# Optimization experiments

Measured on AMD Instinct MI355X. Metric: run time of the kernel, lower is better.

## Reference

```python
import jax, jax.numpy as jnp
import numpy as np

B, I, H, NC, T = 128, 256, 512, 16, 24
M = 14            # max ACT ticks (forward default M=14)
EPS = 0.01        # eps_halting default


def setup_inputs() -> dict:
    key = jax.random.key(0)
    ks = jax.random.split(key, 9)
    s = 1.0 / np.sqrt(H).astype(np.float32)
    u = lambda k, shape: jax.random.uniform(k, shape, jnp.float32, -s, s)
    return {
        "x": jax.random.normal(ks[0], (B, I, T), jnp.float32),
        # LSTMCell params, torch gate order (i, f, g, o)
        "W_ih": u(ks[1], (4 * H, I)),
        "W_hh": u(ks[2], (4 * H, H)),
        "b_ih": u(ks[3], (4 * H,)),
        "b_hh": u(ks[4], (4 * H,)),
        "halt_w": u(ks[5], (1, H)),
        "halt_b": u(ks[6], (1,)),
        "dec_w": u(ks[7], (NC, H)),
        "dec_b": u(ks[8], (NC,)),
    }


def _forward(x, W_ih, W_hh, b_ih, b_hh, halt_w, halt_b, dec_w, dec_b):
    Bn = x.shape[0]
    Hn = W_hh.shape[1]

    def lstm_cell(xi, h, c):
        g = xi @ W_ih.T + b_ih + h @ W_hh.T + b_hh
        i, f, gg, o = jnp.split(g, 4, axis=-1)
        c = jax.nn.sigmoid(f) * c + jax.nn.sigmoid(i) * jnp.tanh(gg)
        h = jax.nn.sigmoid(o) * jnp.tanh(c)
        return h, c

    def act_step(carry, xi):
        # Run M ticks; ACT weighting (ph) zeroes contributions past the halt step,
        # exactly reproducing the torch early-exit semantics.
        def tick(sc, _):
            h, c = lstm_cell(xi, sc[0], sc[1])
            pn = jax.nn.sigmoid(h @ halt_w.T + halt_b)[:, 0]  # [B]
            y = h @ dec_w.T + dec_b                            # [B, NC]
            return (h, c), (pn, h, c, y)

        _, (p_hist, s_hist, c_hist, y_hist) = jax.lax.scan(tick, carry, None, length=M)
        # p_hist [M,B]; s/c_hist [M,B,H]; y_hist [M,B,NC]
        pt_cum = jnp.cumsum(p_hist, axis=0)                    # [M,B]
        all_halted = jnp.all(pt_cum >= 1.0 - EPS, axis=1)      # [M]
        n_stop = jnp.where(jnp.any(all_halted), jnp.argmax(all_halted) + 1, M)
        idx = jnp.arange(M)[:, None]
        # torch: p_max = min(1, cumsum); p_max[:, -1] = 1.0 (last executed tick)
        p_max = jnp.where(idx >= n_stop - 1, 1.0, jnp.minimum(1.0, pt_cum))
        ph = jnp.concatenate([p_max[:1], jnp.diff(p_max, axis=0)], axis=0)  # [M,B]
        st = jnp.einsum('mb,mbh->bh', ph, s_hist)
        ct = jnp.einsum('mb,mbh->bh', ph, c_hist)
        yt = jnp.einsum('mb,mbc->bc', ph, y_hist)
        nt = jnp.argmax(p_max, axis=0)                         # [B] first tick hitting 1.0
        rt = 1.0 - p_max[nt - 1, jnp.arange(Bn)]               # negative index wraps like torch
        pt = nt.astype(x.dtype) + rt
        return (st, ct), (yt, pt, nt)

    z = jnp.zeros((Bn, Hn), x.dtype)
    _, (Y, P, N) = jax.lax.scan(act_step, (z, z), jnp.moveaxis(x, -1, 0))
    Y = jnp.moveaxis(Y, 0, -1)     # [B, NC, T]
    P = jnp.sum(P, axis=0)         # [B]
    N = N.T                        # [B, T]
    return Y, P, N


def reference(x, W_ih, W_hh, b_ih, b_hh, halt_w, halt_b, dec_w, dec_b):
    return _forward(x, W_ih, W_hh, b_ih, b_hh, halt_w, halt_b, dec_w, dec_b)
```

## Files before the change

kernel.cpp:

```cpp
#include <hip/hip_runtime.h>
#include <math.h>

#define NWG 256
#define TPB 1024

static constexpr int Bc=128, Ic=256, Hc=512, NCc=16, Tc=24, Mc=14;
static constexpr int Y_SZ  = Bc*NCc*Tc;
static constexpr int P_OFF = Y_SZ;
static constexpr int N_OFF = Y_SZ + Bc;

static constexpr int HSZ    = Hc*Bc;
static constexpr int HB_OFF = 0;
static constexpr int SC_OFF = 2*HSZ;
static constexpr int HP_OFF = 4*HSZ;
static constexpr int DP_OFF = HP_OFF + 2*2048;

typedef float f4v __attribute__((ext_vector_type(4)));

__device__ __align__(64) unsigned g_bcnt[16][16];
__device__ __align__(64) unsigned g_bgen[16][16];
__device__ __align__(64) unsigned g_brc[16];
__device__ __align__(64) unsigned g_brg[16];

__device__ __forceinline__ float sigm(float v){ return 1.0f/(1.0f+expf(-v)); }

__device__ __forceinline__ void gstore(float* p, float v){
  __hip_atomic_store(p, v, __ATOMIC_RELAXED, __HIP_MEMORY_SCOPE_SYSTEM);
}
__device__ __forceinline__ float gload(const float* p){
  return *(const volatile float*)p;
}

__device__ __forceinline__ void gsync(int w){
  __syncthreads();
  if (threadIdx.x == 0) {
    asm volatile("" ::: "memory");
    const int g = w >> 4;
    unsigned prev = __hip_atomic_fetch_add(&g_bcnt[g][0], 1u, __ATOMIC_RELAXED, __HIP_MEMORY_SCOPE_SYSTEM);
    unsigned ep   = prev >> 4;
    if ((prev & 15u) == 15u) {
      unsigned rprev = __hip_atomic_fetch_add(&g_brc[0], 1u, __ATOMIC_RELAXED, __HIP_MEMORY_SCOPE_SYSTEM);
      if ((rprev & 15u) == 15u) {
        __hip_atomic_store(&g_brg[0], (rprev >> 4) + 1u, __ATOMIC_RELEASE, __HIP_MEMORY_SCOPE_SYSTEM);
      } else {
        while ((int)(__hip_atomic_load(&g_brg[0], __ATOMIC_RELAXED, __HIP_MEMORY_SCOPE_SYSTEM) - (ep + 1u)) < 0)
          __builtin_amdgcn_s_sleep(1);
      }
      __hip_atomic_store(&g_bgen[g][0], ep + 1u, __ATOMIC_RELEASE, __HIP_MEMORY_SCOPE_SYSTEM);
    } else {
      while ((int)(__hip_atomic_load(&g_bgen[g][0], __ATOMIC_RELAXED, __HIP_MEMORY_SCOPE_SYSTEM) - (ep + 1u)) < 0)
        __builtin_amdgcn_s_sleep(1);
    }
    asm volatile("" ::: "memory");
  }
  __syncthreads();
}

__global__ __launch_bounds__(TPB, 1) void act_lstm_kernel(
    const float* __restrict__ x,   const float* __restrict__ Wih,
    const float* __restrict__ Whh, const float* __restrict__ bih,
    const float* __restrict__ bhh, const float* __restrict__ hw,
    const float* __restrict__ hbp, const float* __restrict__ dw,
    const float* __restrict__ db,  float* __restrict__ out,
    float* __restrict__ ws)
{
  const int w    = blockIdx.x;
  const int tid  = threadIdx.x;
  const int lane = tid & 63;
  const int wid  = __builtin_amdgcn_readfirstlane(tid >> 6);
  const int bg   = w >> 4;
  const int js   = w & 15;
  const int kg   = wid;
  const int rl0  = lane, rl1 = lane + 64;
  const int grow0 = ((rl0>>5)<<9) + js*32 + (rl0&31);
  const int grow1 = ((rl1>>5)<<9) + js*32 + (rl1&31);
  const bool iscell = (tid < 256);
  const int jloc = tid >> 3, bl = tid & 7;
  const int jglob = js*32 + jloc;
  const int bglob = bg*8 + bl;

  float* hbuf = ws + HB_OFF;
  float* stc  = ws + SC_OFF;
  float* hpp  = ws + HP_OFF;
  float* decp = ws + DP_OFF;

  __shared__ float h_lds[4096];
  __shared__ float x_lds[2048];
  __shared__ float part[128*129];
  __shared__ float sums[1024];
  __shared__ float dp[4096];
  __shared__ float hp[256];
  __shared__ float pmh[128];
  __shared__ float hq[2048];
  __shared__ float pnl[128];
  __shared__ float dy[2048];
  __shared__ unsigned ldsu[2];

  const f4v* Wh0 = (const f4v*)(Whh + grow0*Hc) + kg*8;
  const f4v* Wh1 = (const f4v*)(Whh + grow1*Hc) + kg*8;
  const f4v* Wx0 = (const f4v*)(Wih + grow0*Ic) + kg*4;
  const f4v* Wx1 = (const f4v*)(Wih + grow1*Ic) + kg*4;

  float bsum[4] = {0,0,0,0};
  float hwj = 0.f;
  if (iscell) {
    #pragma unroll
    for (int g=0; g<4; ++g) bsum[g] = bih[g*512 + jglob] + bhh[g*512 + jglob];
    hwj = hw[jglob];
  }
  const float hb0 = hbp[0];

  float c = 0.f, st_run = 0.f, ct_run = 0.f, prev_pm = 0.f;
  float cumw=0.f, prevw=0.f, ntfw=0.f, rtvw=0.f, psumw=0.f;
  bool  ntsetw = false;
  int   gt = 0, lastpar = 0, pend_t = -1, pend_par = 0;
  float xg[4] = {0,0,0,0};

  for (int t = 0; t < Tc; ++t) {
    for (int mm = 0;; ++mm) {
      const bool do_h = !(mm == 0 && t == 0);
      float xv0 = 0.f, xv1 = 0.f;
      if (mm == 0) {
        const int i0 = tid >> 3, b0 = tid & 7;
        const int xb = (bg*8 + b0) * (Ic*Tc);
        xv0 = x[xb + i0*Tc + t];
        xv1 = x[xb + (i0+128)*Tc + t];
      }
      if (do_h) {
        const float* src = (mm == 0) ? (stc + lastpar*HSZ) : (hbuf + ((gt-1)&1)*HSZ);
        const int j = tid >> 1, q = tid & 1;
        f4v hv = *(const volatile f4v*)(src + j*128 + bg*8 + q*4);
        *(f4v*)&h_lds[tid*4] = hv;
      }
      __syncthreads();

      if (mm == 0) {
        x_lds[tid]        = xv0;
        x_lds[tid + 1024] = xv1;
        __syncthreads();
        float a0[8] = {0,0,0,0,0,0,0,0}, a1[8] = {0,0,0,0,0,0,0,0};
        #pragma unroll
        for (int c4 = 0; c4 < 4; ++c4) {
          f4v w0 = Wx0[c4], w1 = Wx1[c4];
          #pragma unroll
          for (int d = 0; d < 4; ++d) {
            const float wa = w0[d], wb = w1[d];
            const float* hbp_ = &x_lds[(kg*16 + c4*4 + d)*8];
            f4v hA = *(const f4v*)hbp_, hB = *(const f4v*)(hbp_+4);
            a0[0]=fmaf(wa,hA.x,a0[0]); a0[1]=fmaf(wa,hA.y,a0[1]);
            a0[2]=fmaf(wa,hA.z,a0[2]); a0[3]=fmaf(wa,hA.w,a0[3]);
            a0[4]=fmaf(wa,hB.x,a0[4]); a0[5]=fmaf(wa,hB.y,a0[5]);
            a0[6]=fmaf(wa,hB.z,a0[6]); a0[7]=fmaf(wa,hB.w,a0[7]);
            a1[0]=fmaf(wb,hA.x,a1[0]); a1[1]=fmaf(wb,hA.y,a1[1]);
            a1[2]=fmaf(wb,hA.z,a1[2]); a1[3]=fmaf(wb,hA.w,a1[3]);
            a1[4]=fmaf(wb,hB.x,a1[4]); a1[5]=fmaf(wb,hB.y,a1[5]);
            a1[6]=fmaf(wb,hB.z,a1[6]); a1[7]=fmaf(wb,hB.w,a1[7]);
          }
        }
        #pragma unroll
        for (int b = 0; b < 8; ++b) {
          part[rl0*129 + kg*8 + b] = a0[b];
          part[rl1*129 + kg*8 + b] = a1[b];
        }
        __syncthreads();
        {
          const int row = tid >> 3, b = tid & 7;
          float s = 0.f;
          #pragma unroll
          for (int q2 = 0; q2 < 16; ++q2) s += part[row*129 + q2*8 + b];
          sums[tid] = s;
        }
        __syncthreads();
        if (iscell) {
          #pragma unroll
          for (int g = 0; g < 4; ++g) xg[g] = bsum[g] + sums[(g*32 + jloc)*8 + bl];
        }
        __syncthreads();
      }

      {
        float a0[8] = {0,0,0,0,0,0,0,0}, a1[8] = {0,0,0,0,0,0,0,0};
        if (do_h) {
          #pragma unroll
          for (int c4 = 0; c4 < 8; ++c4) {
            f4v w0 = Wh0[c4], w1 = Wh1[c4];
            #pragma unroll
            for (int d = 0; d < 4; ++d) {
              const float wa = w0[d], wb = w1[d];
              const float* hbp_ = &h_lds[(kg*32 + c4*4 + d)*8];
              f4v hA = *(const f4v*)hbp_, hB = *(const f4v*)(hbp_+4);
              a0[0]=fmaf(wa,hA.x,a0[0]); a0[1]=fmaf(wa,hA.y,a0[1]);
              a0[2]=fmaf(wa,hA.z,a0[2]); a0[3]=fmaf(wa,hA.w,a0[3]);
              a0[4]=fmaf(wa,hB.x,a0[4]); a0[5]=fmaf(wa,hB.y,a0[5]);
              a0[6]=fmaf(wa,hB.z,a0[6]); a0[7]=fmaf(wa,hB.w,a0[7]);
              a1[0]=fmaf(wb,hA.x,a1[0]); a1[1]=fmaf(wb,hA.y,a1[1]);
              a1[2]=fmaf(wb,hA.z,a1[2]); a1[3]=fmaf(wb,hA.w,a1[3]);
              a1[4]=fmaf(wb,hB.x,a1[4]); a1[5]=fmaf(wb,hB.y,a1[5]);
              a1[6]=fmaf(wb,hB.z,a1[6]); a1[7]=fmaf(wb,hB.w,a1[7]);
            }
          }
        }
        #pragma unroll
        for (int b = 0; b < 8; ++b) {
          part[rl0*129 + kg*8 + b] = a0[b];
          part[rl1*129 + kg*8 + b] = a1[b];
        }
      }
      __syncthreads();
      {
        const int row = tid >> 3, b = tid & 7;
        float s = 0.f;
        #pragma unroll
        for (int q2 = 0; q2 < 16; ++q2) s += part[row*129 + q2*8 + b];
        sums[tid] = s;
      }
      __syncthreads();

      float hn = 0.f, cn = 0.f;
      if (iscell) {
        float g0 = xg[0] + sums[(0*32 + jloc)*8 + bl];
        float g1 = xg[1] + sums[(1*32 + jloc)*8 + bl];
        float g2 = xg[2] + sums[(2*32 + jloc)*8 + bl];
        float g3 = xg[3] + sums[(3*32 + jloc)*8 + bl];
        float ig = sigm(g0), fg = sigm(g1), gg = tanhf(g2), og = sigm(g3);
        cn = fg*c + ig*gg;
        hn = og*tanhf(cn);
        const int par = gt & 1;
        gstore(hbuf + par*HSZ + jglob*128 + bglob, hn);
        gstore(stc  + par*HSZ + jglob*128 + bglob, st_run + (1.f - prev_pm)*hn);
        hp[tid] = hn * hwj;
      }
      __syncthreads();
      if (tid < 8) {
        float s = 0.f;
        #pragma unroll
        for (int jl = 0; jl < 32; ++jl) s += hp[jl*8 + tid];
        gstore(hpp + (gt&1)*2048 + js*128 + bg*8 + tid, s);
      }

      gsync(w);

      if (pend_t >= 0) {
        if (js == 0) {
          if (tid < 512) {
            const int js2 = tid >> 5, nc = (tid >> 1) & 15, hf = tid & 1;
            f4v v = *(const volatile f4v*)(decp + pend_par*32768 + js2*2048 + nc*128 + bg*8 + hf*4);
            *(f4v*)&dy[js2*128 + nc*8 + hf*4] = v;
          }
          __syncthreads();
          if (tid < 128) {
            const int nc = tid >> 3, b2 = tid & 7;
            float y = 0.f;
            #pragma unroll
            for (int js2 = 0; js2 < 16; ++js2) y += dy[js2*128 + nc*8 + b2];
            out[((bg*8 + b2)*NCc + nc)*Tc + pend_t] = y + db[nc];
          }
        }
        pend_t = -1;
      }
      const int par = gt & 1;
      if (tid < 512) {
        f4v v = *(const volatile f4v*)(hpp + par*2048 + tid*4);
        *(f4v*)&hq[tid*4] = v;
      }
      __syncthreads();
      if (tid < 128) {
        float s = 0.f;
        #pragma unroll
        for (int js2 = 0; js2 < 16; ++js2) s += hq[js2*128 + tid];
        pnl[tid] = s;
      }
      __syncthreads();
      if (wid < 2) {
        const int b2 = wid*64 + lane;
        float pn = sigm(pnl[b2] + hb0);
        cumw += pn;
        int ok = __all(cumw >= 0.99f) ? 1 : 0;
        if (lane == 0) ldsu[wid] = (unsigned)ok;
        pmh[b2] = fminf(1.f, cumw);
      }
      __syncthreads();
      const int finv = (((ldsu[0] & ldsu[1]) != 0u) || (mm == Mc-1)) ? 1 : 0;

      if (wid < 2) {
        float pmf = finv ? 1.f : fminf(1.f, cumw);
        if (!ntsetw && pmf >= 1.f) {
          ntfw = (float)mm;
          rtvw = (mm == 0) ? 0.f : (1.f - prevw);
          ntsetw = true;
        }
        prevw = pmf;
      }
      if (iscell) {
        float pm = finv ? 1.f : pmh[bglob];
        float ph = pm - prev_pm;
        st_run += ph*hn;
        ct_run += ph*cn;
        prev_pm = pm;
        c = finv ? ct_run : cn;
      }
      if (finv) {
        if (iscell) {
          #pragma unroll
          for (int nc = 0; nc < 16; ++nc)
            dp[nc*256 + tid] = dw[nc*512 + jglob] * st_run;
        }
        __syncthreads();
        if (tid < 128) {
          const int nc = tid >> 3, b2 = tid & 7;
          float s = 0.f;
          #pragma unroll
          for (int jl = 0; jl < 32; ++jl) s += dp[nc*256 + jl*8 + b2];
          gstore(decp + par*32768 + js*2048 + nc*128 + bg*8 + b2, s);
        }
        if (w == 0 && wid < 2)
          out[N_OFF + (wid*64 + lane)*Tc + t] = ntfw;
        if (wid < 2) {
          psumw += ntfw + rtvw;
          ntsetw = false; prevw = 0.f; cumw = 0.f; ntfw = 0.f; rtvw = 0.f;
        }
        if (iscell) { st_run = 0.f; ct_run = 0.f; prev_pm = 0.f; }
        pend_t = t; pend_par = par; lastpar = par;
      }
      ++gt;
      if (finv) break;
    }
  }

  gsync(w);
  if (pend_t >= 0 && js == 0) {
    if (tid < 512) {
      const int js2 = tid >> 5, nc = (tid >> 1) & 15, hf = tid & 1;
      f4v v = *(const volatile f4v*)(decp + pend_par*32768 + js2*2048 + nc*128 + bg*8 + hf*4);
      *(f4v*)&dy[js2*128 + nc*8 + hf*4] = v;
    }
    __syncthreads();
    if (tid < 128) {
      const int nc = tid >> 3, b2 = tid & 7;
      float y = 0.f;
      #pragma unroll
      for (int js2 = 0; js2 < 16; ++js2) y += dy[js2*128 + nc*8 + b2];
      out[((bg*8 + b2)*NCc + nc)*Tc + pend_t] = y + db[nc];
    }
  }
  if (w == 1 && wid < 2) out[P_OFF + wid*64 + lane] = psumw;
}

extern "C" void kernel_launch(void* const* d_in, const int* in_sizes, int n_in,
                              void* d_out, int out_size, void* d_ws, size_t ws_size,
                              hipStream_t stream) {
  const float* x   = (const float*)d_in[0];
  const float* Wih = (const float*)d_in[1];
  const float* Whh = (const float*)d_in[2];
  const float* bih = (const float*)d_in[3];
  const float* bhh = (const float*)d_in[4];
  const float* hw  = (const float*)d_in[5];
  const float* hb  = (const float*)d_in[6];
  const float* dwp = (const float*)d_in[7];
  const float* dbp = (const float*)d_in[8];
  float* out = (float*)d_out;
  float* ws  = (float*)d_ws;

  void* kargs[] = {(void*)&x, (void*)&Wih, (void*)&Whh, (void*)&bih, (void*)&bhh,
                   (void*)&hw, (void*)&hb, (void*)&dwp, (void*)&dbp, (void*)&out, (void*)&ws};
  hipLaunchCooperativeKernel((void*)act_lstm_kernel, dim3(NWG), dim3(TPB),
                             kargs, 0, stream);
}
```

Before: 1.998 ms.

## Remap workgroups across XCDs, prefetch hidden state after barrier, distribute decoder reduction

Changes the workgroup-to-(batch group, column slice) mapping so that consecutive block IDs, which land on different XCDs, spread the column slices across dies. Right after the grid barrier, each block loads the freshly written hidden-state slice into a register and reuses it as the next tick's h input, which removes the separate global load at the top of the next tick. The deferred decoder output reduction is now split so every block sums only its own class across the 16 column partials, instead of block js==0 reducing all 16 classes. This spreads the reduction work and removes one __syncthreads on that path, at the cost of an extra global read per tick that is wasted when the step halts.

```diff
diff --git a/kernel.cpp b/kernel.cpp
--- a/kernel.cpp
+++ b/kernel.cpp
@@ -68,8 +68,9 @@
   const int tid  = threadIdx.x;
   const int lane = tid & 63;
   const int wid  = __builtin_amdgcn_readfirstlane(tid >> 6);
-  const int bg   = w >> 4;
-  const int js   = w & 15;
+  const int xcg  = w & 7, xidx = w >> 3;
+  const int js   = (xcg << 1) | (xidx & 1);
+  const int bg   = xidx >> 1;
   const int kg   = wid;
   const int rl0  = lane, rl1 = lane + 64;
   const int grow0 = ((rl0>>5)<<9) + js*32 + (rl0&31);
@@ -93,7 +94,7 @@
   __shared__ float pmh[128];
   __shared__ float hq[2048];
   __shared__ float pnl[128];
-  __shared__ float dy[2048];
+  __shared__ float dy[128];
   __shared__ unsigned ldsu[2];
 
   const f4v* Wh0 = (const f4v*)(Whh + grow0*Hc) + kg*8;
@@ -115,6 +116,8 @@
   bool  ntsetw = false;
   int   gt = 0, lastpar = 0, pend_t = -1, pend_par = 0;
   float xg[4] = {0,0,0,0};
+  f4v   spec = {0,0,0,0};
+  bool  have_spec = false;
 
   for (int t = 0; t < Tc; ++t) {
     for (int mm = 0;; ++mm) {
@@ -127,10 +130,14 @@
         xv1 = x[xb + (i0+128)*Tc + t];
       }
       if (do_h) {
-        const float* src = (mm == 0) ? (stc + lastpar*HSZ) : (hbuf + ((gt-1)&1)*HSZ);
-        const int j = tid >> 1, q = tid & 1;
-        f4v hv = *(const volatile f4v*)(src + j*128 + bg*8 + q*4);
-        *(f4v*)&h_lds[tid*4] = hv;
+        if (mm > 0 && have_spec) {
+          *(f4v*)&h_lds[tid*4] = spec;
+        } else {
+          const float* src = (mm == 0) ? (stc + lastpar*HSZ) : (hbuf + ((gt-1)&1)*HSZ);
+          const int j = tid >> 1, q = tid & 1;
+          f4v hv = *(const volatile f4v*)(src + j*128 + bg*8 + q*4);
+          *(f4v*)&h_lds[tid*4] = hv;
+        }
       }
       __syncthreads();
 
@@ -240,28 +247,19 @@
 
       gsync(w);
 
-      if (pend_t >= 0) {
-        if (js == 0) {
-          if (tid < 512) {
-            const int js2 = tid >> 5, nc = (tid >> 1) & 15, hf = tid & 1;
-            f4v v = *(const volatile f4v*)(decp + pend_par*32768 + js2*2048 + nc*128 + bg*8 + hf*4);
-            *(f4v*)&dy[js2*128 + nc*8 + hf*4] = v;
-          }
-          __syncthreads();
-          if (tid < 128) {
-            const int nc = tid >> 3, b2 = tid & 7;
-            float y = 0.f;
-            #pragma unroll
-            for (int js2 = 0; js2 < 16; ++js2) y += dy[js2*128 + nc*8 + b2];
-            out[((bg*8 + b2)*NCc + nc)*Tc + pend_t] = y + db[nc];
-          }
-        }
-        pend_t = -1;
-      }
       const int par = gt & 1;
+      {
+        const int j = tid >> 1, q = tid & 1;
+        spec = *(const volatile f4v*)(hbuf + par*HSZ + j*128 + bg*8 + q*4);
+        have_spec = true;
+      }
       if (tid < 512) {
         f4v v = *(const volatile f4v*)(hpp + par*2048 + tid*4);
         *(f4v*)&hq[tid*4] = v;
+      } else if (pend_t >= 0 && tid < 544) {
+        const int js2 = (tid - 512) >> 1, hf = tid & 1;
+        f4v v = *(const volatile f4v*)(decp + pend_par*32768 + js2*2048 + js*128 + bg*8 + hf*4);
+        *(f4v*)&dy[js2*8 + hf*4] = v;
       }
       __syncthreads();
       if (tid < 128) {
@@ -269,8 +267,16 @@
         #pragma unroll
         for (int js2 = 0; js2 < 16; ++js2) s += hq[js2*128 + tid];
         pnl[tid] = s;
-      }
-      __syncthreads();
+      } else if (pend_t >= 0 && tid >= 256 && tid < 264) {
+        const int b2 = tid - 256;
+        float y = 0.f;
+        #pragma unroll
+        for (int js2 = 0; js2 < 16; ++js2) y += dy[js2*8 + b2];
+        out[((bg*8 + b2)*NCc + js)*Tc + pend_t] = y + db[js];
+      }
+      if (pend_t >= 0 && tid == 0) ;
+      __syncthreads();
+      pend_t = -1;
       if (wid < 2) {
         const int b2 = wid*64 + lane;
         float pn = sigm(pnl[b2] + hb0);
@@ -313,7 +319,7 @@
           for (int jl = 0; jl < 32; ++jl) s += dp[nc*256 + jl*8 + b2];
           gstore(decp + par*32768 + js*2048 + nc*128 + bg*8 + b2, s);
         }
-        if (w == 0 && wid < 2)
+        if (bg == 0 && js == 0 && wid < 2)
           out[N_OFF + (wid*64 + lane)*Tc + t] = ntfw;
         if (wid < 2) {
           psumw += ntfw + rtvw;
@@ -328,22 +334,21 @@
   }
 
   gsync(w);
-  if (pend_t >= 0 && js == 0) {
-    if (tid < 512) {
-      const int js2 = tid >> 5, nc = (tid >> 1) & 15, hf = tid & 1;
-      f4v v = *(const volatile f4v*)(decp + pend_par*32768 + js2*2048 + nc*128 + bg*8 + hf*4);
-      *(f4v*)&dy[js2*128 + nc*8 + hf*4] = v;
+  if (pend_t >= 0) {
+    if (tid < 32) {
+      const int js2 = tid >> 1, hf = tid & 1;
+      f4v v = *(const volatile f4v*)(decp + pend_par*32768 + js2*2048 + js*128 + bg*8 + hf*4);
+      *(f4v*)&dy[js2*8 + hf*4] = v;
     }
     __syncthreads();
-    if (tid < 128) {
-      const int nc = tid >> 3, b2 = tid & 7;
+    if (tid < 8) {
       float y = 0.f;
       #pragma unroll
-      for (int js2 = 0; js2 < 16; ++js2) y += dy[js2*128 + nc*8 + b2];
-      out[((bg*8 + b2)*NCc + nc)*Tc + pend_t] = y + db[nc];
+      for (int js2 = 0; js2 < 16; ++js2) y += dy[js2*8 + tid];
+      out[((bg*8 + tid)*NCc + js)*Tc + pend_t] = y + db[js];
     }
   }
-  if (w == 1 && wid < 2) out[P_OFF + wid*64 + lane] = psumw;
+  if (bg == 0 && js == 1 && wid < 2) out[P_OFF + wid*64 + lane] = psumw;
 }
 
 extern "C" void kernel_launch(void* const* d_in, const int* in_sizes, int n_in,
```

New measurement: 1.929 ms. 3.5% less time.
